# Kernel tuning notes

Hardware: AMD Instinct MI355X
Metric: run time of the kernel (lower is better)

The kernel has to match this reference:

```python
import jax, jax.numpy as jnp
import numpy as np

N_HEAD = 8
LN_EPS = 1e-5


def _layer_norm(x, g, b):
    mu = jnp.mean(x, axis=-1, keepdims=True)
    var = jnp.mean(jnp.square(x - mu), axis=-1, keepdims=True)
    return (x - mu) * jax.lax.rsqrt(var + LN_EPS) * g + b


def _pos_encoding(L, d, dtype):
    pos = jnp.arange(L, dtype=jnp.float32)[:, None]                      # [L,1]
    div = jnp.exp(jnp.arange(0, d, 2, dtype=jnp.float32) * (-np.log(10000.0) / d))  # [d/2]
    # interleave sin (even idx) / cos (odd idx)
    pe = jnp.stack([jnp.sin(pos * div), jnp.cos(pos * div)], axis=-1).reshape(L, d)
    return pe.astype(dtype)


def setup_inputs() -> dict:
    key = jax.random.key(0)
    B, L, D, F, NL = 256, 100, 512, 2048, 4
    ks = jax.random.split(key, 8)
    s = lambda fan_in: 1.0 / np.sqrt(fan_in)
    return {
        "x": jax.random.normal(ks[0], (B, L, D), dtype=jnp.float32),
        "mask": jnp.ones((B, L), dtype=jnp.int32),
        # weights stored as [in, out] (torch Linear weight transposed)
        "qkv_w": jax.random.uniform(ks[1], (NL, D, 3 * D), minval=-s(D), maxval=s(D)),
        "fc_w": jax.random.uniform(ks[2], (NL, D, D), minval=-s(D), maxval=s(D)),
        "fc_b": jnp.zeros((NL, D), dtype=jnp.float32),
        "ln1_g": jnp.ones((NL, D), dtype=jnp.float32),
        "ln1_b": jnp.zeros((NL, D), dtype=jnp.float32),
        "ln2_g": jnp.ones((NL, D), dtype=jnp.float32),
        "ln2_b": jnp.zeros((NL, D), dtype=jnp.float32),
        "ffn_w1": jax.random.uniform(ks[3], (NL, D, F), minval=-s(D), maxval=s(D)),
        "ffn_b1": jnp.zeros((NL, F), dtype=jnp.float32),
        "ffn_w2": jax.random.uniform(ks[4], (NL, F, D), minval=-s(F), maxval=s(F)),
        "ffn_b2": jnp.zeros((NL, D), dtype=jnp.float32),
    }


def _attn(x, mask, qkv_w, fc_w, fc_b):
    B, L, D = x.shape
    hd = D // N_HEAD
    qkv = x @ qkv_w                                      # [B,L,3D]
    q, k, v = jnp.split(qkv, 3, axis=-1)
    q = q.reshape(B, L, N_HEAD, hd).transpose(0, 2, 1, 3)   # [B,H,L,hd]
    k = k.reshape(B, L, N_HEAD, hd).transpose(0, 2, 1, 3)
    v = v.reshape(B, L, N_HEAD, hd).transpose(0, 2, 1, 3)
    scores = jnp.einsum("bhqd,bhkd->bhqk", q, k)          # scale=1 (scale=False)
    scores = jnp.where(mask[:, None, None, :] == 0, -jnp.inf, scores)
    attn = jax.nn.softmax(scores, axis=-1)
    out = jnp.einsum("bhqk,bhkd->bhqd", attn, v)
    out = out.transpose(0, 2, 1, 3).reshape(B, L, D)
    return out @ fc_w + fc_b


def reference(x, mask, qkv_w, fc_w, fc_b, ln1_g, ln1_b, ln2_g, ln2_b,
              ffn_w1, ffn_b1, ffn_w2, ffn_b2):
    B, L, D = x.shape
    pe = _pos_encoding(L, D, x.dtype)                     # [L,D]
    # pos_embed: x = x + (x + pe)  (dropout is identity at eval)
    x = x + (x + pe[None, :, :])
    n_layers = qkv_w.shape[0]
    for i in range(n_layers):  # post-norm (after_norm=True)
        res = x
        x = _attn(x, mask, qkv_w[i], fc_w[i], fc_b[i])
        x = _layer_norm(x + res, ln1_g[i], ln1_b[i])
        res = x
        h = jax.nn.relu(x @ ffn_w1[i] + ffn_b1[i])
        x = _layer_norm(res + (h @ ffn_w2[i] + ffn_b2[i]), ln2_g[i], ln2_b[i])
    return x
```

## Files before the change

### kernel.cpp

```cpp
#include <hip/hip_runtime.h>
#include <cstdint>
#include <cmath>


#define NLAYERS 4
#define BB 256
#define LL 100
#define DD 512
#define FF 2048
#define NH 8
#define HD 64
#define MM (BB*LL)
#define ATT_R 112
#define ATT_K 128

typedef __bf16 bf16;
typedef bf16 bf16x8 __attribute__((ext_vector_type(8)));
typedef bf16 bf16x4 __attribute__((ext_vector_type(4)));
typedef float f32x4 __attribute__((ext_vector_type(4)));

__device__ __forceinline__ void load16(const void* g, void* l) {
  __builtin_amdgcn_global_load_lds(
      (const __attribute__((address_space(1))) void*)g,
      (__attribute__((address_space(3))) void*)l, 16, 0, 0);
}

__global__ void pe_kernel(float* __restrict__ pe) {
  const int idx = blockIdx.x * 256 + threadIdx.x;
  if (idx >= LL * DD) return;
  const int l = idx >> 9, d = idx & 511;
  const int i = d >> 1;
  const float div = expf((float)(2 * i) * (-9.210340371976184f / 512.f));
  const float ang = (float)l * div;
  pe[idx] = (d & 1) ? cosf(ang) : sinf(ang);
}

__global__ __launch_bounds__(256) void x0_kernel(
    const float* __restrict__ xin, const float* __restrict__ pe,
    bf16* __restrict__ XB) {
  const size_t f = (size_t)blockIdx.x * 256 + threadIdx.x;
  const size_t e = f << 2;
  const int col  = (int)(e & 511);
  const int prow = (int)((e >> 9) % LL);
  const float4 xv = *(const float4*)(xin + e);
  const float4 pv = *(const float4*)(pe + (size_t)prow * DD + col);
  bf16x4 pk;
  pk[0] = (bf16)(2.f * xv.x + pv.x);
  pk[1] = (bf16)(2.f * xv.y + pv.y);
  pk[2] = (bf16)(2.f * xv.z + pv.z);
  pk[3] = (bf16)(2.f * xv.w + pv.w);
  *(bf16x4*)(XB + e) = pk;
}

__global__ void transpose_cast(const float* __restrict__ src, bf16* __restrict__ dst,
                               int K, int N) {
  __shared__ float tile[32][33];
  const int z = blockIdx.z;
  src += (size_t)z * K * N;
  dst += (size_t)z * K * N;
  const int k0 = blockIdx.y * 32, n0 = blockIdx.x * 32;
  const int tx = threadIdx.x, ty = threadIdx.y;
  #pragma unroll
  for (int i = 0; i < 32; i += 8)
    tile[ty + i][tx] = src[(size_t)(k0 + ty + i) * N + n0 + tx];
  __syncthreads();
  #pragma unroll
  for (int i = 0; i < 32; i += 8)
    dst[(size_t)(n0 + ty + i) * K + k0 + tx] = (bf16)tile[tx][ty + i];
}


__device__ __forceinline__ void stage_chunk(const bf16* __restrict__ src, int ldk,
                                            int grow0, int kt, bf16* chunk,
                                            int tid, int w) {
  const int rr = tid >> 3;
  const int cb = (tid & 7) ^ (rr & 7);
  const bf16* g = src + (size_t)(grow0 + rr) * ldk + (kt << 6) + (cb << 3);
  load16(g, chunk + (w << 9));
  load16(g + ((size_t)ldk << 6), chunk + 4096 + (w << 9));
}

__device__ __forceinline__ bf16x8 lds_frag(const bf16* chunk, int lrow, int cb) {
  return *(const bf16x8*)(chunk + (lrow << 6) + ((cb ^ (lrow & 7)) << 3));
}

template<int OUT_BF16, int RELU>
__global__ __launch_bounds__(512) void gemm256(
    const bf16* __restrict__ A, const bf16* __restrict__ Bt,
    const float* __restrict__ bias, void* __restrict__ Cv,
    int N, int K) {
  __shared__ __align__(16) bf16 sA[2][2][128 * 64];
  __shared__ __align__(16) bf16 sB[2][2][128 * 64];
  const int tid = threadIdx.x;
  const int w = tid >> 6, lane = tid & 63;
  const int wr = w >> 2, wc = w & 3;
  const int lr16 = lane & 15, lg = lane >> 4;
  const int NT = K >> 6;

  const int nwg = gridDim.x * gridDim.y;
  const int orig = blockIdx.y * gridDim.x + blockIdx.x;
  const int q = nwg >> 3, r = nwg & 7;
  const int xcd = orig & 7, lo = orig >> 3;
  const int swz = (xcd < r ? xcd * (q + 1) : r * (q + 1) + (xcd - r) * q) + lo;
  const int bn = (swz % gridDim.x) << 8;
  const int bm = (swz / gridDim.x) << 8;

  f32x4 acc[8][4] = {};
  bf16x8 Av[4][2], Bv0[2][2], Bv1[2][2];

  stage_chunk(A,  K, bm,       0, sA[0][0], tid, w);
  stage_chunk(Bt, K, bn,       0, sB[0][0], tid, w);
  stage_chunk(A,  K, bm + 128, 0, sA[0][1], tid, w);
  stage_chunk(Bt, K, bn + 128, 0, sB[0][1], tid, w);
  stage_chunk(A,  K, bm,       1, sA[1][0], tid, w);
  stage_chunk(Bt, K, bn,       1, sB[1][0], tid, w);

  for (int t = 0; t < NT; ++t) {
    const int b = t & 1;
    if (t < NT - 1) asm volatile("s_waitcnt vmcnt(4)" ::: "memory");
    else            asm volatile("s_waitcnt vmcnt(0)" ::: "memory");
    __builtin_amdgcn_s_barrier();

    #pragma unroll
    for (int m = 0; m < 4; ++m) {
      const int lrow = m * 32 + wr * 16 + lr16;
      Av[m][0] = lds_frag(sA[b][0], lrow, lg);
      Av[m][1] = lds_frag(sA[b][0], lrow, 4 + lg);
    }
    #pragma unroll
    for (int n = 0; n < 2; ++n) {
      const int lrow = n * 64 + wc * 16 + lr16;
      Bv0[n][0] = lds_frag(sB[b][0], lrow, lg);
      Bv0[n][1] = lds_frag(sB[b][0], lrow, 4 + lg);
    }
    if (t + 1 < NT) stage_chunk(A, K, bm + 128, t + 1, sA[b ^ 1][1], tid, w);
    __builtin_amdgcn_s_barrier();
    __builtin_amdgcn_s_setprio(1);
    #pragma unroll
    for (int m = 0; m < 4; ++m)
      #pragma unroll
      for (int n = 0; n < 2; ++n) {
        acc[m][n] = __builtin_amdgcn_mfma_f32_16x16x32_bf16(Av[m][0], Bv0[n][0], acc[m][n], 0, 0, 0);
        acc[m][n] = __builtin_amdgcn_mfma_f32_16x16x32_bf16(Av[m][1], Bv0[n][1], acc[m][n], 0, 0, 0);
      }
    __builtin_amdgcn_s_setprio(0);
    __builtin_amdgcn_s_barrier();

    #pragma unroll
    for (int n = 0; n < 2; ++n) {
      const int lrow = n * 64 + wc * 16 + lr16;
      Bv1[n][0] = lds_frag(sB[b][1], lrow, lg);
      Bv1[n][1] = lds_frag(sB[b][1], lrow, 4 + lg);
    }
    if (t + 1 < NT) stage_chunk(Bt, K, bn + 128, t + 1, sB[b ^ 1][1], tid, w);
    __builtin_amdgcn_s_barrier();
    __builtin_amdgcn_s_setprio(1);
    #pragma unroll
    for (int m = 0; m < 4; ++m)
      #pragma unroll
      for (int n = 0; n < 2; ++n) {
        acc[m][n + 2] = __builtin_amdgcn_mfma_f32_16x16x32_bf16(Av[m][0], Bv1[n][0], acc[m][n + 2], 0, 0, 0);
        acc[m][n + 2] = __builtin_amdgcn_mfma_f32_16x16x32_bf16(Av[m][1], Bv1[n][1], acc[m][n + 2], 0, 0, 0);
      }
    __builtin_amdgcn_s_setprio(0);
    __builtin_amdgcn_s_barrier();

    #pragma unroll
    for (int m = 0; m < 4; ++m) {
      const int lrow = m * 32 + wr * 16 + lr16;
      Av[m][0] = lds_frag(sA[b][1], lrow, lg);
      Av[m][1] = lds_frag(sA[b][1], lrow, 4 + lg);
    }
    if (t + 2 < NT) stage_chunk(A, K, bm, t + 2, sA[b][0], tid, w);
    __builtin_amdgcn_s_barrier();
    __builtin_amdgcn_s_setprio(1);
    #pragma unroll
    for (int m = 0; m < 4; ++m)
      #pragma unroll
      for (int n = 0; n < 2; ++n) {
        acc[m + 4][n] = __builtin_amdgcn_mfma_f32_16x16x32_bf16(Av[m][0], Bv0[n][0], acc[m + 4][n], 0, 0, 0);
        acc[m + 4][n] = __builtin_amdgcn_mfma_f32_16x16x32_bf16(Av[m][1], Bv0[n][1], acc[m + 4][n], 0, 0, 0);
      }
    __builtin_amdgcn_s_setprio(0);
    __builtin_amdgcn_s_barrier();

    if (t + 2 < NT) stage_chunk(Bt, K, bn, t + 2, sB[b][0], tid, w);
    __builtin_amdgcn_s_barrier();
    __builtin_amdgcn_s_setprio(1);
    #pragma unroll
    for (int m = 0; m < 4; ++m)
      #pragma unroll
      for (int n = 0; n < 2; ++n) {
        acc[m + 4][n + 2] = __builtin_amdgcn_mfma_f32_16x16x32_bf16(Av[m][0], Bv1[n][0], acc[m + 4][n + 2], 0, 0, 0);
        acc[m + 4][n + 2] = __builtin_amdgcn_mfma_f32_16x16x32_bf16(Av[m][1], Bv1[n][1], acc[m + 4][n + 2], 0, 0, 0);
      }
    __builtin_amdgcn_s_setprio(0);
  }

  const int g4 = (lane >> 4) << 2;
  #pragma unroll
  for (int n = 0; n < 4; ++n) {
    const int col = bn + n * 64 + wc * 16 + lr16;
    const float bvv = bias ? bias[col] : 0.f;
    #pragma unroll
    for (int m = 0; m < 8; ++m) {
      const int row = bm + m * 32 + wr * 16 + g4;
      #pragma unroll
      for (int j = 0; j < 4; ++j) {
        float v = acc[m][n][j] + bvv;
        if (RELU) v = fmaxf(v, 0.f);
        if (OUT_BF16) ((bf16*)Cv)[(size_t)(row + j) * N + col] = (bf16)v;
        else          ((float*)Cv)[(size_t)(row + j) * N + col] = v;
      }
    }
  }
}

__global__ __launch_bounds__(256) void attn_mfma(
    const bf16* __restrict__ qkv, const int* __restrict__ mask,
    bf16* __restrict__ aout) {
  __shared__ __align__(16) bf16 sQ[ATT_R * 64];
  __shared__ __align__(16) bf16 sK[ATT_R * 64];
  __shared__ __align__(16) bf16 sVt[64 * 136];
  __shared__ __align__(16) bf16 sP[ATT_R * ATT_K];
  __shared__ int sM[ATT_R];
  const int bh = blockIdx.x, b = bh >> 3, h = bh & 7;
  const int tid = threadIdx.x, w = tid >> 6, lane = tid & 63;
  const int lr = lane & 15;
  const int lk = (lane >> 4) << 3;
  const int g  = lane >> 4;

  for (int i = tid; i < ATT_R * 64 / 8; i += 256) { ((int4*)sQ)[i] = int4{0,0,0,0}; ((int4*)sK)[i] = int4{0,0,0,0}; }
  for (int i = tid; i < 64 * 136 / 8; i += 256) ((int4*)sVt)[i] = int4{0,0,0,0};
  for (int i = tid; i < ATT_R * ATT_K / 8; i += 256) ((int4*)sP)[i] = int4{0,0,0,0};
  __syncthreads();

  const bf16* base = qkv + (size_t)(b * LL) * (3 * DD) + h * HD;
  for (int c = tid; c < LL * 8; c += 256) {
    const int l = c >> 3, u = c & 7;
    const bf16x8 qv = *(const bf16x8*)(base + (size_t)l * (3 * DD) + u * 8);
    const bf16x8 kv = *(const bf16x8*)(base + (size_t)l * (3 * DD) + DD + u * 8);
    const bf16x8 vv = *(const bf16x8*)(base + (size_t)l * (3 * DD) + 2 * DD + u * 8);
    const int qb = (l * 128 + u * 16) ^ ((l & 7) << 4);
    *(bf16x8*)((char*)sQ + qb) = qv;
    *(bf16x8*)((char*)sK + qb) = kv;
    #pragma unroll
    for (int j = 0; j < 8; ++j) sVt[(u * 8 + j) * 136 + l] = vv[j];
  }
  if (tid < ATT_R) sM[tid] = (tid < LL) ? mask[b * LL + tid] : 0;
  __syncthreads();

  #pragma unroll
  for (int fi = 0; fi < 2; ++fi) {
    const int fm = w + fi * 4;
    if (fm >= 7) continue;
    const int ar = fm * 16 + lr;
    const int abase = ar * 128;
    const int aswz = (ar & 7) << 4;
    const bf16x8 a0 = *(const bf16x8*)((char*)sQ + ((abase + lk * 2) ^ aswz));
    const bf16x8 a1 = *(const bf16x8*)((char*)sQ + ((abase + 64 + lk * 2) ^ aswz));
    f32x4 s[7];
    #pragma unroll
    for (int fn = 0; fn < 7; ++fn) {
      const int br = fn * 16 + lr;
      const int bswz = (br & 7) << 4;
      const bf16x8 b0 = *(const bf16x8*)((char*)sK + ((br * 128 + lk * 2) ^ bswz));
      const bf16x8 b1 = *(const bf16x8*)((char*)sK + ((br * 128 + 64 + lk * 2) ^ bswz));
      f32x4 acc = {};
      acc = __builtin_amdgcn_mfma_f32_16x16x32_bf16(a0, b0, acc, 0, 0, 0);
      acc = __builtin_amdgcn_mfma_f32_16x16x32_bf16(a1, b1, acc, 0, 0, 0);
      s[fn] = acc;
    }
    #pragma unroll
    for (int fn = 0; fn < 7; ++fn) {
      if (sM[fn * 16 + lr] == 0) {
        s[fn][0] = -INFINITY; s[fn][1] = -INFINITY;
        s[fn][2] = -INFINITY; s[fn][3] = -INFINITY;
      }
    }
    float sm[4];
    #pragma unroll
    for (int j = 0; j < 4; ++j) {
      float m = s[0][j];
      #pragma unroll
      for (int fn = 1; fn < 7; ++fn) m = fmaxf(m, s[fn][j]);
      #pragma unroll
      for (int off = 1; off < 16; off <<= 1) m = fmaxf(m, __shfl_xor(m, off, 64));
      float t = 0.f;
      #pragma unroll
      for (int fn = 0; fn < 7; ++fn) { const float p = __expf(s[fn][j] - m); s[fn][j] = p; t += p; }
      #pragma unroll
      for (int off = 1; off < 16; off <<= 1) t += __shfl_xor(t, off, 64);
      sm[j] = 1.f / t;
    }
    #pragma unroll
    for (int fn = 0; fn < 7; ++fn) {
      const int k = fn * 16 + lr;
      #pragma unroll
      for (int j = 0; j < 4; ++j) {
        const int rr = fm * 16 + 4 * g + j;
        const int byte = (rr * 256 + k * 2) ^ ((rr & 7) << 4);
        *(bf16*)((char*)sP + byte) = (bf16)(s[fn][j] * sm[j]);
      }
    }
  }
  __syncthreads();

  bf16x8 bV[4];
  #pragma unroll
  for (int ks = 0; ks < 4; ++ks)
    bV[ks] = *(const bf16x8*)((char*)sVt + ((w * 16 + lr) * 272 + ks * 64 + lk * 2));
  #pragma unroll
  for (int fm = 0; fm < 7; ++fm) {
    f32x4 acc = {};
    const int ar = fm * 16 + lr;
    const int aswz = (ar & 7) << 4;
    #pragma unroll
    for (int ks = 0; ks < 4; ++ks) {
      const bf16x8 aP = *(const bf16x8*)((char*)sP + ((ar * 256 + ks * 64 + lk * 2) ^ aswz));
      acc = __builtin_amdgcn_mfma_f32_16x16x32_bf16(aP, bV[ks], acc, 0, 0, 0);
    }
    const int d = h * HD + w * 16 + lr;
    #pragma unroll
    for (int j = 0; j < 4; ++j) {
      const int qr = fm * 16 + 4 * g + j;
      if (qr < LL) aout[(size_t)(b * LL + qr) * DD + d] = (bf16)acc[j];
    }
  }
}

template<int WRITE_F32>
__global__ __launch_bounds__(64) void ln_kernel(
    const float* __restrict__ Y, const bf16* __restrict__ RES,
    const float* __restrict__ g, const float* __restrict__ bt,
    bf16* __restrict__ XB, float* __restrict__ XF) {
  const int row = blockIdx.x;
  const int lane = threadIdx.x;
  const size_t base = (size_t)row * DD + lane * 8;
  const float4 a0 = *(const float4*)(Y + base);
  const float4 a1 = *(const float4*)(Y + base + 4);
  const bf16x8 rv = *(const bf16x8*)(RES + base);
  float z[8];
  z[0] = a0.x + (float)rv[0]; z[1] = a0.y + (float)rv[1];
  z[2] = a0.z + (float)rv[2]; z[3] = a0.w + (float)rv[3];
  z[4] = a1.x + (float)rv[4]; z[5] = a1.y + (float)rv[5];
  z[6] = a1.z + (float)rv[6]; z[7] = a1.w + (float)rv[7];
  float s = 0.f, s2 = 0.f;
  #pragma unroll
  for (int j = 0; j < 8; ++j) { s += z[j]; s2 = fmaf(z[j], z[j], s2); }
  #pragma unroll
  for (int off = 32; off > 0; off >>= 1) {
    s  += __shfl_xor(s, off, 64);
    s2 += __shfl_xor(s2, off, 64);
  }
  const float mu = s * (1.f / 512.f);
  const float var = s2 * (1.f / 512.f) - mu * mu;
  const float inv = rsqrtf(var + 1e-5f);
  const int c = lane * 8;
  const float4 g0 = *(const float4*)(g + c),  g1 = *(const float4*)(g + c + 4);
  const float4 b0 = *(const float4*)(bt + c), b1 = *(const float4*)(bt + c + 4);
  float ov[8];
  ov[0] = (z[0] - mu) * inv * g0.x + b0.x; ov[1] = (z[1] - mu) * inv * g0.y + b0.y;
  ov[2] = (z[2] - mu) * inv * g0.z + b0.z; ov[3] = (z[3] - mu) * inv * g0.w + b0.w;
  ov[4] = (z[4] - mu) * inv * g1.x + b1.x; ov[5] = (z[5] - mu) * inv * g1.y + b1.y;
  ov[6] = (z[6] - mu) * inv * g1.z + b1.z; ov[7] = (z[7] - mu) * inv * g1.w + b1.w;
  bf16x8 pk;
  #pragma unroll
  for (int j = 0; j < 8; ++j) pk[j] = (bf16)ov[j];
  *(bf16x8*)(XB + base) = pk;
  if (WRITE_F32) {
    *(float4*)(XF + base)     = make_float4(ov[0], ov[1], ov[2], ov[3]);
    *(float4*)(XF + base + 4) = make_float4(ov[4], ov[5], ov[6], ov[7]);
  }
}

extern "C" void kernel_launch(void* const* d_in, const int* in_sizes, int n_in,
                              void* d_out, int out_size, void* d_ws, size_t ws_size,
                              hipStream_t stream) {
  const float* x_in   = (const float*)d_in[0];
  const int*   mask   = (const int*)d_in[1];
  const float* qkv_w  = (const float*)d_in[2];
  const float* fc_w   = (const float*)d_in[3];
  const float* fc_b   = (const float*)d_in[4];
  const float* ln1_g  = (const float*)d_in[5];
  const float* ln1_b  = (const float*)d_in[6];
  const float* ln2_g  = (const float*)d_in[7];
  const float* ln2_b  = (const float*)d_in[8];
  const float* ffn_w1 = (const float*)d_in[9];
  const float* ffn_b1 = (const float*)d_in[10];
  const float* ffn_w2 = (const float*)d_in[11];
  const float* ffn_b2 = (const float*)d_in[12];

  char* ws = (char*)d_ws;
  size_t off = 0;
  auto alloc = [&](size_t bytes) -> void* {
    off = (off + 255) & ~(size_t)255;
    void* p = ws + off;
    off += bytes;
    return p;
  };
  bf16*  XB   = (bf16*) alloc((size_t)MM * DD * 2);
  bf16*  BIGB = (bf16*) alloc((size_t)MM * FF * 2);
  float* PE   = (float*)alloc((size_t)LL * DD * 4);
  bf16*  WQKV = (bf16*) alloc((size_t)NLAYERS * DD * 3 * DD * 2);
  bf16*  WFC  = (bf16*) alloc((size_t)NLAYERS * DD * DD * 2);
  bf16*  W1T  = (bf16*) alloc((size_t)NLAYERS * DD * FF * 2);
  bf16*  W2T  = (bf16*) alloc((size_t)NLAYERS * FF * DD * 2);
  bf16*  AOUT = BIGB + (size_t)MM * (3 * DD);
  float* Y    = (float*)d_out;
  (void)ws_size; (void)in_sizes; (void)n_in; (void)out_size;

  pe_kernel<<<200, 256, 0, stream>>>(PE);
  transpose_cast<<<dim3(48, 16, NLAYERS), dim3(32, 8), 0, stream>>>(qkv_w,  WQKV, 512, 1536);
  transpose_cast<<<dim3(16, 16, NLAYERS), dim3(32, 8), 0, stream>>>(fc_w,   WFC,  512, 512);
  transpose_cast<<<dim3(64, 16, NLAYERS), dim3(32, 8), 0, stream>>>(ffn_w1, W1T,  512, 2048);
  transpose_cast<<<dim3(16, 64, NLAYERS), dim3(32, 8), 0, stream>>>(ffn_w2, W2T,  2048, 512);
  x0_kernel<<<12800, 256, 0, stream>>>(x_in, PE, XB);

  for (int i = 0; i < NLAYERS; ++i) {
    gemm256<1, 0><<<dim3(6, 100), 512, 0, stream>>>(
        XB, WQKV + (size_t)i * DD * 3 * DD, nullptr, BIGB, 3 * DD, DD);
    attn_mfma<<<BB * NH, 256, 0, stream>>>(BIGB, mask, AOUT);
    gemm256<0, 0><<<dim3(2, 100), 512, 0, stream>>>(
        AOUT, WFC + (size_t)i * DD * DD, fc_b + i * DD, Y, DD, DD);
    ln_kernel<0><<<MM, 64, 0, stream>>>(Y, XB, ln1_g + i * DD, ln1_b + i * DD, XB, nullptr);
    gemm256<1, 1><<<dim3(8, 100), 512, 0, stream>>>(
        XB, W1T + (size_t)i * DD * FF, ffn_b1 + i * FF, BIGB, FF, DD);
    gemm256<0, 0><<<dim3(2, 100), 512, 0, stream>>>(
        BIGB, W2T + (size_t)i * FF * DD, ffn_b2 + i * DD, Y, DD, FF);
    if (i == NLAYERS - 1)
      ln_kernel<1><<<MM, 64, 0, stream>>>(Y, XB, ln2_g + i * DD, ln2_b + i * DD,
                                          XB, (float*)d_out);
    else
      ln_kernel<0><<<MM, 64, 0, stream>>>(Y, XB, ln2_g + i * DD, ln2_b + i * DD, XB, nullptr);
  }
}
```

Baseline: 1.236 ms.

## Add 128x128 tiled GEMM for N=512 projections and batch LN rows per block

Adds a gemm128 kernel with 128x128 tiles, 256 threads, double-buffered LDS staging and an XCD-aware block swizzle. It is used for the fc and FFN-down GEMMs (N=512), which launched only 200 blocks with the 256-wide tile and underfilled the GPU. The LayerNorm kernel now handles four rows per 256-thread block instead of one row per 64-thread block, to cut launch and scheduling overhead. Smaller tiles mean less reuse per loaded byte and more total global traffic for A and B.

Result: slower. 1.315 ms (+6.4%).

```diff
diff --git a/kernel.cpp b/kernel.cpp
--- a/kernel.cpp
+++ b/kernel.cpp
@@ -69,7 +69,6 @@
     dst[(size_t)(n0 + ty + i) * K + k0 + tx] = (bf16)tile[tx][ty + i];
 }
 
-
 __device__ __forceinline__ void stage_chunk(const bf16* __restrict__ src, int ldk,
                                             int grow0, int kt, bf16* chunk,
                                             int tid, int w) {
@@ -208,6 +207,156 @@
       #pragma unroll
       for (int j = 0; j < 4; ++j) {
         float v = acc[m][n][j] + bvv;
+        if (RELU) v = fmaxf(v, 0.f);
+        if (OUT_BF16) ((bf16*)Cv)[(size_t)(row + j) * N + col] = (bf16)v;
+        else          ((float*)Cv)[(size_t)(row + j) * N + col] = v;
+      }
+    }
+  }
+}
+
+__device__ __forceinline__ void stage64(const bf16*& pa, const bf16*& pb,
+                                        bf16* dst, int w) {
+  load16(pa, dst + (w << 9));
+  load16(pb, dst + 2048 + (w << 9));
+  pa += 64; pb += 64;
+}
+
+template<int OUT_BF16, int RELU>
+__global__ __launch_bounds__(256, 2) void gemm128(
+    const bf16* __restrict__ A, const bf16* __restrict__ Bt,
+    const float* __restrict__ bias, void* __restrict__ Cv,
+    int N, int K) {
+  __shared__ __align__(16) bf16 sA[2][2][64 * 64];
+  __shared__ __align__(16) bf16 sB[2][2][64 * 64];
+  const int tid = threadIdx.x;
+  const int w = tid >> 6, lane = tid & 63;
+  const int wr = w >> 1, wc = w & 1;
+  const int lr16 = lane & 15, lg = lane >> 4;
+  const int NT = K >> 6;
+
+  const int nwg = gridDim.x * gridDim.y;
+  const int orig = blockIdx.y * gridDim.x + blockIdx.x;
+  const int q = nwg >> 3, r = nwg & 7;
+  const int xcd = orig & 7, lo = orig >> 3;
+  const int swz = (xcd < r ? xcd * (q + 1) : r * (q + 1) + (xcd - r) * q) + lo;
+  const int bn = (swz % gridDim.x) << 7;
+  const int bm = (swz / gridDim.x) << 7;
+
+  auto mksrc = [&](const bf16* base, int grow0, int i) -> const bf16* {
+    const int p = i * 256 + tid;
+    const int prow = p >> 3;
+    const int cbl = (p & 7) ^ (prow & 7);
+    return base + (size_t)(grow0 + prow) * K + (cbl << 3);
+  };
+  const bf16* pA0a = mksrc(A, bm, 0);        const bf16* pA0b = mksrc(A, bm, 1);
+  const bf16* pA1a = mksrc(A, bm + 64, 0);   const bf16* pA1b = mksrc(A, bm + 64, 1);
+  const bf16* pB0a = mksrc(Bt, bn, 0);       const bf16* pB0b = mksrc(Bt, bn, 1);
+  const bf16* pB1a = mksrc(Bt, bn + 64, 0);  const bf16* pB1b = mksrc(Bt, bn + 64, 1);
+
+  f32x4 acc[4][4] = {};
+  bf16x8 Am[2][2], Bn0[2][2], Bn1[2][2];
+
+  stage64(pA0a, pA0b, sA[0][0], w);
+  stage64(pB0a, pB0b, sB[0][0], w);
+  stage64(pA1a, pA1b, sA[0][1], w);
+  stage64(pB1a, pB1b, sB[0][1], w);
+  stage64(pA0a, pA0b, sA[1][0], w);
+  stage64(pB0a, pB0b, sB[1][0], w);
+
+  for (int t = 0; t < NT; ++t) {
+    const int b = t & 1;
+    if (t < NT - 1) asm volatile("s_waitcnt vmcnt(4)" ::: "memory");
+    else            asm volatile("s_waitcnt vmcnt(0)" ::: "memory");
+    __builtin_amdgcn_s_barrier();
+
+    #pragma unroll
+    for (int m = 0; m < 2; ++m) {
+      const int lrow = m * 32 + wr * 16 + lr16;
+      Am[m][0] = lds_frag(sA[b][0], lrow, lg);
+      Am[m][1] = lds_frag(sA[b][0], lrow, 4 + lg);
+    }
+    #pragma unroll
+    for (int n = 0; n < 2; ++n) {
+      const int lrow = n * 32 + wc * 16 + lr16;
+      Bn0[n][0] = lds_frag(sB[b][0], lrow, lg);
+      Bn0[n][1] = lds_frag(sB[b][0], lrow, 4 + lg);
+    }
+    if (t + 1 < NT) stage64(pA1a, pA1b, sA[b ^ 1][1], w);
+    __builtin_amdgcn_s_barrier();
+    __builtin_amdgcn_s_setprio(1);
+    #pragma unroll
+    for (int m = 0; m < 2; ++m)
+      #pragma unroll
+      for (int n = 0; n < 2; ++n) {
+        acc[m][n] = __builtin_amdgcn_mfma_f32_16x16x32_bf16(Am[m][0], Bn0[n][0], acc[m][n], 0, 0, 0);
+        acc[m][n] = __builtin_amdgcn_mfma_f32_16x16x32_bf16(Am[m][1], Bn0[n][1], acc[m][n], 0, 0, 0);
+      }
+    __builtin_amdgcn_s_setprio(0);
+    __builtin_amdgcn_s_barrier();
+
+    #pragma unroll
+    for (int n = 0; n < 2; ++n) {
+      const int lrow = n * 32 + wc * 16 + lr16;
+      Bn1[n][0] = lds_frag(sB[b][1], lrow, lg);
+      Bn1[n][1] = lds_frag(sB[b][1], lrow, 4 + lg);
+    }
+    if (t + 1 < NT) stage64(pB1a, pB1b, sB[b ^ 1][1], w);
+    __builtin_amdgcn_s_barrier();
+    __builtin_amdgcn_s_setprio(1);
+    #pragma unroll
+    for (int m = 0; m < 2; ++m)
+      #pragma unroll
+      for (int n = 0; n < 2; ++n) {
+        acc[m][n + 2] = __builtin_amdgcn_mfma_f32_16x16x32_bf16(Am[m][0], Bn1[n][0], acc[m][n + 2], 0, 0, 0);
+        acc[m][n + 2] = __builtin_amdgcn_mfma_f32_16x16x32_bf16(Am[m][1], Bn1[n][1], acc[m][n + 2], 0, 0, 0);
+      }
+    __builtin_amdgcn_s_setprio(0);
+    __builtin_amdgcn_s_barrier();
+
+    #pragma unroll
+    for (int m = 0; m < 2; ++m) {
+      const int lrow = m * 32 + wr * 16 + lr16;
+      Am[m][0] = lds_frag(sA[b][1], lrow, lg);
+      Am[m][1] = lds_frag(sA[b][1], lrow, 4 + lg);
+    }
+    if (t + 2 < NT) stage64(pA0a, pA0b, sA[b][0], w);
+    __builtin_amdgcn_s_barrier();
+    __builtin_amdgcn_s_setprio(1);
+    #pragma unroll
+    for (int m = 0; m < 2; ++m)
+      #pragma unroll
+      for (int n = 0; n < 2; ++n) {
+        acc[m + 2][n] = __builtin_amdgcn_mfma_f32_16x16x32_bf16(Am[m][0], Bn0[n][0], acc[m + 2][n], 0, 0, 0);
+        acc[m + 2][n] = __builtin_amdgcn_mfma_f32_16x16x32_bf16(Am[m][1], Bn0[n][1], acc[m + 2][n], 0, 0, 0);
+      }
+    __builtin_amdgcn_s_setprio(0);
+    __builtin_amdgcn_s_barrier();
+
+    if (t + 2 < NT) stage64(pB0a, pB0b, sB[b][0], w);
+    __builtin_amdgcn_s_barrier();
+    __builtin_amdgcn_s_setprio(1);
+    #pragma unroll
+    for (int m = 0; m < 2; ++m)
+      #pragma unroll
+      for (int n = 0; n < 2; ++n) {
+        acc[m + 2][n + 2] = __builtin_amdgcn_mfma_f32_16x16x32_bf16(Am[m][0], Bn1[n][0], acc[m + 2][n + 2], 0, 0, 0);
+        acc[m + 2][n + 2] = __builtin_amdgcn_mfma_f32_16x16x32_bf16(Am[m][1], Bn1[n][1], acc[m + 2][n + 2], 0, 0, 0);
+      }
+    __builtin_amdgcn_s_setprio(0);
+  }
+
+  const int g4 = (lane >> 4) << 2;
+  #pragma unroll
+  for (int ni = 0; ni < 4; ++ni) {
+    const int col = bn + (ni >> 1) * 64 + (ni & 1) * 32 + wc * 16 + lr16;
+    const float bvv = bias ? bias[col] : 0.f;
+    #pragma unroll
+    for (int mi = 0; mi < 4; ++mi) {
+      const int row = bm + (mi >> 1) * 64 + (mi & 1) * 32 + wr * 16 + g4;
+      #pragma unroll
+      for (int j = 0; j < 4; ++j) {
+        float v = acc[mi][ni][j] + bvv;
         if (RELU) v = fmaxf(v, 0.f);
         if (OUT_BF16) ((bf16*)Cv)[(size_t)(row + j) * N + col] = (bf16)v;
         else          ((float*)Cv)[(size_t)(row + j) * N + col] = v;
@@ -330,12 +479,12 @@
 }
 
 template<int WRITE_F32>
-__global__ __launch_bounds__(64) void ln_kernel(
+__global__ __launch_bounds__(256) void ln_kernel(
     const float* __restrict__ Y, const bf16* __restrict__ RES,
     const float* __restrict__ g, const float* __restrict__ bt,
     bf16* __restrict__ XB, float* __restrict__ XF) {
-  const int row = blockIdx.x;
-  const int lane = threadIdx.x;
+  const int row = blockIdx.x * 4 + (threadIdx.x >> 6);
+  const int lane = threadIdx.x & 63;
   const size_t base = (size_t)row * DD + lane * 8;
   const float4 a0 = *(const float4*)(Y + base);
   const float4 a1 = *(const float4*)(Y + base + 4);
@@ -421,17 +570,17 @@
     gemm256<1, 0><<<dim3(6, 100), 512, 0, stream>>>(
         XB, WQKV + (size_t)i * DD * 3 * DD, nullptr, BIGB, 3 * DD, DD);
     attn_mfma<<<BB * NH, 256, 0, stream>>>(BIGB, mask, AOUT);
-    gemm256<0, 0><<<dim3(2, 100), 512, 0, stream>>>(
+    gemm128<0, 0><<<dim3(4, 200), 256, 0, stream>>>(
         AOUT, WFC + (size_t)i * DD * DD, fc_b + i * DD, Y, DD, DD);
-    ln_kernel<0><<<MM, 64, 0, stream>>>(Y, XB, ln1_g + i * DD, ln1_b + i * DD, XB, nullptr);
+    ln_kernel<0><<<MM / 4, 256, 0, stream>>>(Y, XB, ln1_g + i * DD, ln1_b + i * DD, XB, nullptr);
     gemm256<1, 1><<<dim3(8, 100), 512, 0, stream>>>(
         XB, W1T + (size_t)i * DD * FF, ffn_b1 + i * FF, BIGB, FF, DD);
-    gemm256<0, 0><<<dim3(2, 100), 512, 0, stream>>>(
+    gemm128<0, 0><<<dim3(4, 200), 256, 0, stream>>>(
         BIGB, W2T + (size_t)i * FF * DD, ffn_b2 + i * DD, Y, DD, FF);
     if (i == NLAYERS - 1)
-      ln_kernel<1><<<MM, 64, 0, stream>>>(Y, XB, ln2_g + i * DD, ln2_b + i * DD,
-                                          XB, (float*)d_out);
+      ln_kernel<1><<<MM / 4, 256, 0, stream>>>(Y, XB, ln2_g + i * DD, ln2_b + i * DD,
+                                               XB, (float*)d_out);
     else
-      ln_kernel<0><<<MM, 64, 0, stream>>>(Y, XB, ln2_g + i * DD, ln2_b + i * DD, XB, nullptr);
-  }
-}
+      ln_kernel<0><<<MM / 4, 256, 0, stream>>>(Y, XB, ln2_g + i * DD, ln2_b + i * DD, XB, nullptr);
+  }
+}
```

## Fuse output-projection and FFN2 GEMMs with residual add and LayerNorm

Applied to the files above, without the earlier changes.

Adds a gemm_ln kernel in which each 512-thread block computes a full 128x512 row tile, so it owns every column of its rows and can apply bias, residual add and LayerNorm in its epilogue. This replaces the fp32 Y round trip and the separate ln_kernel launches after the fc and ffn_w2 GEMMs. In exchange, only 200 blocks are launched for these GEMMs, which may underfill the GPU. The epilogue reads and writes XB in place, which is safe only because each block touches just its own rows. A dead extra LDS load was also added in attention, which is probably harmless.

Result: slower. 1.396 ms (+13.0%).

```diff
diff --git a/kernel.cpp b/kernel.cpp
--- a/kernel.cpp
+++ b/kernel.cpp
@@ -69,7 +69,6 @@
     dst[(size_t)(n0 + ty + i) * K + k0 + tx] = (bf16)tile[tx][ty + i];
 }
 
-
 __device__ __forceinline__ void stage_chunk(const bf16* __restrict__ src, int ldk,
                                             int grow0, int kt, bf16* chunk,
                                             int tid, int w) {
@@ -211,6 +210,169 @@
         if (RELU) v = fmaxf(v, 0.f);
         if (OUT_BF16) ((bf16*)Cv)[(size_t)(row + j) * N + col] = (bf16)v;
         else          ((float*)Cv)[(size_t)(row + j) * N + col] = v;
+      }
+    }
+  }
+}
+
+template<int WRITE_F32>
+__global__ __launch_bounds__(512) void gemm_ln(
+    const bf16* __restrict__ A, const bf16* __restrict__ Bt,
+    const float* __restrict__ bias, const bf16* __restrict__ RES,
+    const float* __restrict__ lng, const float* __restrict__ lnb,
+    bf16* __restrict__ XB, float* __restrict__ XF, int K) {
+  __shared__ __align__(16) bf16 sA[2][128 * 32];
+  __shared__ __align__(16) bf16 sB[2][512 * 32];
+  const int tid = threadIdx.x;
+  const int w = tid >> 6, lane = tid & 63;
+  const int wc = w;
+  const int lr16 = lane & 15, lg = lane >> 4;
+  const int NT = K >> 5;
+
+  const int q = gridDim.x >> 3;
+  const int swz = (blockIdx.x & 7) * q + (blockIdx.x >> 3);
+  const int bm = swz << 7;
+
+  const int rr = tid >> 2;
+  const int cbl = (tid & 3) ^ (rr & 3);
+  const bf16* gA  = A  + (size_t)(bm + rr) * K + (cbl << 3);
+  const bf16* gB0 = Bt + (size_t)(0   + rr) * K + (cbl << 3);
+  const bf16* gB1 = Bt + (size_t)(128 + rr) * K + (cbl << 3);
+  const bf16* gB2 = Bt + (size_t)(256 + rr) * K + (cbl << 3);
+  const bf16* gB3 = Bt + (size_t)(384 + rr) * K + (cbl << 3);
+
+  f32x4 acc[8][4] = {};
+  bf16x8 Af[4], Bf[4];
+
+  load16(gA,       sA[0] + (w << 9));
+  load16(gB0,      sB[0] + 0 * 4096 + (w << 9));
+  load16(gB1,      sB[0] + 1 * 4096 + (w << 9));
+  load16(gB2,      sB[0] + 2 * 4096 + (w << 9));
+  load16(gB3,      sB[0] + 3 * 4096 + (w << 9));
+  load16(gB0 + 32, sB[1] + 0 * 4096 + (w << 9));
+  load16(gB1 + 32, sB[1] + 1 * 4096 + (w << 9));
+  load16(gB2 + 32, sB[1] + 2 * 4096 + (w << 9));
+  load16(gB3 + 32, sB[1] + 3 * 4096 + (w << 9));
+
+  for (int t = 0; t < NT; ++t) {
+    const int pb = t & 1;
+    const bf16* bufA = sA[pb];
+    const bf16* bufB = sB[pb];
+    if (t < NT - 1) asm volatile("s_waitcnt vmcnt(4)" ::: "memory");
+    else            asm volatile("s_waitcnt vmcnt(0)" ::: "memory");
+    __builtin_amdgcn_s_barrier();
+
+    #pragma unroll
+    for (int m = 0; m < 4; ++m) {
+      const int row = m * 16 + lr16;
+      Af[m] = *(const bf16x8*)&bufA[row * 32 + ((lg ^ (row & 3)) << 3)];
+    }
+    #pragma unroll
+    for (int n = 0; n < 4; ++n) {
+      const int row = wc * 64 + n * 16 + lr16;
+      Bf[n] = *(const bf16x8*)&bufB[row * 32 + ((lg ^ (row & 3)) << 3)];
+    }
+    if (t + 1 < NT) load16(gA + (t + 1) * 32, sA[pb ^ 1] + (w << 9));
+    __builtin_amdgcn_s_barrier();
+    __builtin_amdgcn_s_setprio(1);
+    #pragma unroll
+    for (int m = 0; m < 4; ++m)
+      #pragma unroll
+      for (int n = 0; n < 4; ++n)
+        acc[m][n] = __builtin_amdgcn_mfma_f32_16x16x32_bf16(Af[m], Bf[n], acc[m][n], 0, 0, 0);
+    __builtin_amdgcn_s_setprio(0);
+    __builtin_amdgcn_s_barrier();
+
+    #pragma unroll
+    for (int m = 0; m < 4; ++m) {
+      const int row = (m + 4) * 16 + lr16;
+      Af[m] = *(const bf16x8*)&bufA[row * 32 + ((lg ^ (row & 3)) << 3)];
+    }
+    if (t + 2 < NT) {
+      const int ko = (t + 2) * 32;
+      load16(gB0 + ko, sB[pb] + 0 * 4096 + (w << 9));
+      load16(gB1 + ko, sB[pb] + 1 * 4096 + (w << 9));
+      load16(gB2 + ko, sB[pb] + 2 * 4096 + (w << 9));
+      load16(gB3 + ko, sB[pb] + 3 * 4096 + (w << 9));
+    }
+    __builtin_amdgcn_s_barrier();
+    __builtin_amdgcn_s_setprio(1);
+    #pragma unroll
+    for (int m = 0; m < 4; ++m)
+      #pragma unroll
+      for (int n = 0; n < 4; ++n)
+        acc[m + 4][n] = __builtin_amdgcn_mfma_f32_16x16x32_bf16(Af[m], Bf[n], acc[m + 4][n], 0, 0, 0);
+    __builtin_amdgcn_s_setprio(0);
+  }
+
+  __syncthreads();
+  float* redS = (float*)sA;
+  float* muS  = (float*)sB;
+
+  int colv[4];
+  #pragma unroll
+  for (int n = 0; n < 4; ++n) colv[n] = wc * 64 + n * 16 + lr16;
+
+  #pragma unroll
+  for (int m = 0; m < 8; ++m) {
+    #pragma unroll
+    for (int j = 0; j < 4; ++j) {
+      const int row = m * 16 + (lg << 2) + j;
+      const size_t gr = (size_t)(bm + row) * DD;
+      #pragma unroll
+      for (int n = 0; n < 4; ++n)
+        acc[m][n][j] += bias[colv[n]] + (float)RES[gr + colv[n]];
+    }
+  }
+  #pragma unroll
+  for (int m = 0; m < 8; ++m) {
+    #pragma unroll
+    for (int j = 0; j < 4; ++j) {
+      float s  = acc[m][0][j] + acc[m][1][j] + acc[m][2][j] + acc[m][3][j];
+      float s2 = acc[m][0][j] * acc[m][0][j] + acc[m][1][j] * acc[m][1][j]
+               + acc[m][2][j] * acc[m][2][j] + acc[m][3][j] * acc[m][3][j];
+      #pragma unroll
+      for (int off = 1; off < 16; off <<= 1) {
+        s  += __shfl_xor(s, off, 64);
+        s2 += __shfl_xor(s2, off, 64);
+      }
+      if (lr16 == 0) {
+        const int row = m * 16 + (lg << 2) + j;
+        redS[row * 16 + wc * 2]     = s;
+        redS[row * 16 + wc * 2 + 1] = s2;
+      }
+    }
+  }
+  __syncthreads();
+  if (tid < 128) {
+    float s = 0.f, s2 = 0.f;
+    #pragma unroll
+    for (int wv = 0; wv < 8; ++wv) {
+      s  += redS[tid * 16 + wv * 2];
+      s2 += redS[tid * 16 + wv * 2 + 1];
+    }
+    const float mu  = s * (1.f / 512.f);
+    const float var = s2 * (1.f / 512.f) - mu * mu;
+    muS[tid]       = mu;
+    muS[128 + tid] = rsqrtf(var + 1e-5f);
+  }
+  __syncthreads();
+  float gmv[4], btv[4];
+  #pragma unroll
+  for (int n = 0; n < 4; ++n) { gmv[n] = lng[colv[n]]; btv[n] = lnb[colv[n]]; }
+  #pragma unroll
+  for (int m = 0; m < 8; ++m) {
+    #pragma unroll
+    for (int j = 0; j < 4; ++j) {
+      const int row = m * 16 + (lg << 2) + j;
+      const float mu  = muS[row];
+      const float inv = muS[128 + row];
+      const size_t gr = (size_t)(bm + row) * DD;
+      #pragma unroll
+      for (int n = 0; n < 4; ++n) {
+        const float o = (acc[m][n][j] - mu) * inv * gmv[n] + btv[n];
+        XB[gr + colv[n]] = (bf16)o;
+        if (WRITE_F32) XF[gr + colv[n]] = o;
       }
     }
   }
@@ -317,8 +479,10 @@
     const int aswz = (ar & 7) << 4;
     #pragma unroll
     for (int ks = 0; ks < 4; ++ks) {
-      const bf16x8 aP = *(const bf16x8*)((char*)sP + ((ar * 256 + ks * 64 + lk * 2) ^ aswz));
-      acc = __builtin_amdgcn_mfma_f32_16x16x32_bf16(aP, bV[ks], acc, 0, 0, 0);
+      const bf16x8 aP = *(const bf16x8*)((char*)sVt + 0);
+      (void)aP;
+      const bf16x8 aP2 = *(const bf16x8*)((char*)sP + ((ar * 256 + ks * 64 + lk * 2) ^ aswz));
+      acc = __builtin_amdgcn_mfma_f32_16x16x32_bf16(aP2, bV[ks], acc, 0, 0, 0);
     }
     const int d = h * HD + w * 16 + lr;
     #pragma unroll
@@ -326,51 +490,6 @@
       const int qr = fm * 16 + 4 * g + j;
       if (qr < LL) aout[(size_t)(b * LL + qr) * DD + d] = (bf16)acc[j];
     }
-  }
-}
-
-template<int WRITE_F32>
-__global__ __launch_bounds__(64) void ln_kernel(
-    const float* __restrict__ Y, const bf16* __restrict__ RES,
-    const float* __restrict__ g, const float* __restrict__ bt,
-    bf16* __restrict__ XB, float* __restrict__ XF) {
-  const int row = blockIdx.x;
-  const int lane = threadIdx.x;
-  const size_t base = (size_t)row * DD + lane * 8;
-  const float4 a0 = *(const float4*)(Y + base);
-  const float4 a1 = *(const float4*)(Y + base + 4);
-  const bf16x8 rv = *(const bf16x8*)(RES + base);
-  float z[8];
-  z[0] = a0.x + (float)rv[0]; z[1] = a0.y + (float)rv[1];
-  z[2] = a0.z + (float)rv[2]; z[3] = a0.w + (float)rv[3];
-  z[4] = a1.x + (float)rv[4]; z[5] = a1.y + (float)rv[5];
-  z[6] = a1.z + (float)rv[6]; z[7] = a1.w + (float)rv[7];
-  float s = 0.f, s2 = 0.f;
-  #pragma unroll
-  for (int j = 0; j < 8; ++j) { s += z[j]; s2 = fmaf(z[j], z[j], s2); }
-  #pragma unroll
-  for (int off = 32; off > 0; off >>= 1) {
-    s  += __shfl_xor(s, off, 64);
-    s2 += __shfl_xor(s2, off, 64);
-  }
-  const float mu = s * (1.f / 512.f);
-  const float var = s2 * (1.f / 512.f) - mu * mu;
-  const float inv = rsqrtf(var + 1e-5f);
-  const int c = lane * 8;
-  const float4 g0 = *(const float4*)(g + c),  g1 = *(const float4*)(g + c + 4);
-  const float4 b0 = *(const float4*)(bt + c), b1 = *(const float4*)(bt + c + 4);
-  float ov[8];
-  ov[0] = (z[0] - mu) * inv * g0.x + b0.x; ov[1] = (z[1] - mu) * inv * g0.y + b0.y;
-  ov[2] = (z[2] - mu) * inv * g0.z + b0.z; ov[3] = (z[3] - mu) * inv * g0.w + b0.w;
-  ov[4] = (z[4] - mu) * inv * g1.x + b1.x; ov[5] = (z[5] - mu) * inv * g1.y + b1.y;
-  ov[6] = (z[6] - mu) * inv * g1.z + b1.z; ov[7] = (z[7] - mu) * inv * g1.w + b1.w;
-  bf16x8 pk;
-  #pragma unroll
-  for (int j = 0; j < 8; ++j) pk[j] = (bf16)ov[j];
-  *(bf16x8*)(XB + base) = pk;
-  if (WRITE_F32) {
-    *(float4*)(XF + base)     = make_float4(ov[0], ov[1], ov[2], ov[3]);
-    *(float4*)(XF + base + 4) = make_float4(ov[4], ov[5], ov[6], ov[7]);
   }
 }
 
@@ -407,7 +526,6 @@
   bf16*  W1T  = (bf16*) alloc((size_t)NLAYERS * DD * FF * 2);
   bf16*  W2T  = (bf16*) alloc((size_t)NLAYERS * FF * DD * 2);
   bf16*  AOUT = BIGB + (size_t)MM * (3 * DD);
-  float* Y    = (float*)d_out;
   (void)ws_size; (void)in_sizes; (void)n_in; (void)out_size;
 
   pe_kernel<<<200, 256, 0, stream>>>(PE);
@@ -421,17 +539,18 @@
     gemm256<1, 0><<<dim3(6, 100), 512, 0, stream>>>(
         XB, WQKV + (size_t)i * DD * 3 * DD, nullptr, BIGB, 3 * DD, DD);
     attn_mfma<<<BB * NH, 256, 0, stream>>>(BIGB, mask, AOUT);
-    gemm256<0, 0><<<dim3(2, 100), 512, 0, stream>>>(
-        AOUT, WFC + (size_t)i * DD * DD, fc_b + i * DD, Y, DD, DD);
-    ln_kernel<0><<<MM, 64, 0, stream>>>(Y, XB, ln1_g + i * DD, ln1_b + i * DD, XB, nullptr);
+    gemm_ln<0><<<200, 512, 0, stream>>>(
+        AOUT, WFC + (size_t)i * DD * DD, fc_b + i * DD, XB,
+        ln1_g + i * DD, ln1_b + i * DD, XB, nullptr, DD);
     gemm256<1, 1><<<dim3(8, 100), 512, 0, stream>>>(
         XB, W1T + (size_t)i * DD * FF, ffn_b1 + i * FF, BIGB, FF, DD);
-    gemm256<0, 0><<<dim3(2, 100), 512, 0, stream>>>(
-        BIGB, W2T + (size_t)i * FF * DD, ffn_b2 + i * DD, Y, DD, FF);
     if (i == NLAYERS - 1)
-      ln_kernel<1><<<MM, 64, 0, stream>>>(Y, XB, ln2_g + i * DD, ln2_b + i * DD,
-                                          XB, (float*)d_out);
+      gemm_ln<1><<<200, 512, 0, stream>>>(
+          BIGB, W2T + (size_t)i * FF * DD, ffn_b2 + i * DD, XB,
+          ln2_g + i * DD, ln2_b + i * DD, XB, (float*)d_out, FF);
     else
-      ln_kernel<0><<<MM, 64, 0, stream>>>(Y, XB, ln2_g + i * DD, ln2_b + i * DD, XB, nullptr);
-  }
-}
+      gemm_ln<0><<<200, 512, 0, stream>>>(
+          BIGB, W2T + (size_t)i * FF * DD, ffn_b2 + i * DD, XB,
+          ln2_g + i * DD, ln2_b + i * DD, XB, nullptr, FF);
+  }
+}
```

## Add 128x128-tile GEMM with XCD swizzle for N=512 GEMMs, batch LN rows

Applied to the files above, without the earlier changes.

Adds a new gemm128 kernel with 128x128 tiles, 256 threads, double-buffered LDS staging and an XCD-aware block swizzle. It replaces the 256-tile GEMM for the two N=512 projections (attention output fc and FFN down), which launched only 200 workgroups and so under-filled the GPU. The layer-norm kernel now handles four rows per 256-thread block instead of one row per 64-thread block, cutting launch and scheduling overhead. The smaller tiles reuse less data per load and raise total global traffic.

After: 1.199 ms. 1.03x faster.

```diff
diff --git a/kernel.cpp b/kernel.cpp
--- a/kernel.cpp
+++ b/kernel.cpp
@@ -69,7 +69,6 @@
     dst[(size_t)(n0 + ty + i) * K + k0 + tx] = (bf16)tile[tx][ty + i];
 }
 
-
 __device__ __forceinline__ void stage_chunk(const bf16* __restrict__ src, int ldk,
                                             int grow0, int kt, bf16* chunk,
                                             int tid, int w) {
@@ -205,6 +204,105 @@
     #pragma unroll
     for (int m = 0; m < 8; ++m) {
       const int row = bm + m * 32 + wr * 16 + g4;
+      #pragma unroll
+      for (int j = 0; j < 4; ++j) {
+        float v = acc[m][n][j] + bvv;
+        if (RELU) v = fmaxf(v, 0.f);
+        if (OUT_BF16) ((bf16*)Cv)[(size_t)(row + j) * N + col] = (bf16)v;
+        else          ((float*)Cv)[(size_t)(row + j) * N + col] = v;
+      }
+    }
+  }
+}
+
+__device__ __forceinline__ void stage4(const bf16* g, size_t r32, bf16* chunk, int w) {
+  load16(g,            chunk + (w << 9));
+  load16(g + r32,      chunk + 2048 + (w << 9));
+  load16(g + 2 * r32,  chunk + 4096 + (w << 9));
+  load16(g + 3 * r32,  chunk + 6144 + (w << 9));
+}
+
+template<int OUT_BF16, int RELU>
+__global__ __launch_bounds__(256, 2) void gemm128(
+    const bf16* __restrict__ A, const bf16* __restrict__ Bt,
+    const float* __restrict__ bias, void* __restrict__ Cv,
+    int N, int K) {
+  __shared__ __align__(16) bf16 sA[2][128 * 64];
+  __shared__ __align__(16) bf16 sB[2][128 * 64];
+  const int tid = threadIdx.x;
+  const int w = tid >> 6, lane = tid & 63;
+  const int wr = w >> 1, wc = w & 1;
+  const int lr16 = lane & 15, lg = lane >> 4;
+  const int NT = K >> 6;
+
+  const int nwg = gridDim.x * gridDim.y;
+  const int orig = blockIdx.y * gridDim.x + blockIdx.x;
+  const int q = nwg >> 3, r = nwg & 7;
+  const int xcd = orig & 7, lo = orig >> 3;
+  const int swz = (xcd < r ? xcd * (q + 1) : r * (q + 1) + (xcd - r) * q) + lo;
+  const int bn = (swz % gridDim.x) << 7;
+  const int bm = (swz / gridDim.x) << 7;
+
+  const int rr0 = tid >> 3;
+  const int cb  = (tid & 7) ^ (rr0 & 7);
+  const bf16* gA = A  + (size_t)(bm + rr0) * K + (cb << 3);
+  const bf16* gB = Bt + (size_t)(bn + rr0) * K + (cb << 3);
+  const size_t r32 = (size_t)32 * K;
+
+  f32x4 acc[4][4] = {};
+  bf16x8 Af[4][2], Bf[4][2];
+
+  stage4(gA,      r32, sA[0], w);
+  stage4(gB,      r32, sB[0], w);
+  stage4(gA + 64, r32, sA[1], w);
+  stage4(gB + 64, r32, sB[1], w);
+
+  for (int t = 0; t < NT; ++t) {
+    const int cur = t & 1;
+    if (t < NT - 1) asm volatile("s_waitcnt vmcnt(8)" ::: "memory");
+    else            asm volatile("s_waitcnt vmcnt(0)" ::: "memory");
+    __builtin_amdgcn_s_barrier();
+
+    #pragma unroll
+    for (int m = 0; m < 4; ++m) {
+      const int lrow = wr * 64 + m * 16 + lr16;
+      Af[m][0] = lds_frag(sA[cur], lrow, lg);
+      Af[m][1] = lds_frag(sA[cur], lrow, 4 + lg);
+    }
+    #pragma unroll
+    for (int n = 0; n < 4; ++n) {
+      const int lrow = wc * 64 + n * 16 + lr16;
+      Bf[n][0] = lds_frag(sB[cur], lrow, lg);
+      Bf[n][1] = lds_frag(sB[cur], lrow, 4 + lg);
+    }
+    __builtin_amdgcn_s_barrier();
+
+    if (t + 2 < NT) stage4(gA + (size_t)(t + 2) * 64, r32, sA[cur], w);
+    __builtin_amdgcn_s_setprio(1);
+    #pragma unroll
+    for (int m = 0; m < 4; ++m)
+      #pragma unroll
+      for (int n = 0; n < 4; ++n)
+        acc[m][n] = __builtin_amdgcn_mfma_f32_16x16x32_bf16(Af[m][0], Bf[n][0], acc[m][n], 0, 0, 0);
+    __builtin_amdgcn_s_setprio(0);
+    if (t + 2 < NT) stage4(gB + (size_t)(t + 2) * 64, r32, sB[cur], w);
+    __builtin_amdgcn_s_setprio(1);
+    #pragma unroll
+    for (int m = 0; m < 4; ++m)
+      #pragma unroll
+      for (int n = 0; n < 4; ++n)
+        acc[m][n] = __builtin_amdgcn_mfma_f32_16x16x32_bf16(Af[m][1], Bf[n][1], acc[m][n], 0, 0, 0);
+    __builtin_amdgcn_s_setprio(0);
+  }
+
+  const int g4 = (lane >> 4) << 2;
+  #pragma unroll
+  for (int n = 0; n < 4; ++n) {
+    const int col = bn + wc * 64 + n * 16 + lr16;
+    const float bvv = bias ? bias[col] : 0.f;
+    #pragma unroll
+    for (int m = 0; m < 4; ++m) {
+      const int row = bm + wr * 64 + m * 16 + g4;
       #pragma unroll
       for (int j = 0; j < 4; ++j) {
         float v = acc[m][n][j] + bvv;
@@ -330,12 +428,12 @@
 }
 
 template<int WRITE_F32>
-__global__ __launch_bounds__(64) void ln_kernel(
+__global__ __launch_bounds__(256) void ln_kernel(
     const float* __restrict__ Y, const bf16* __restrict__ RES,
     const float* __restrict__ g, const float* __restrict__ bt,
     bf16* __restrict__ XB, float* __restrict__ XF) {
-  const int row = blockIdx.x;
-  const int lane = threadIdx.x;
+  const int row = blockIdx.x * 4 + (threadIdx.x >> 6);
+  const int lane = threadIdx.x & 63;
   const size_t base = (size_t)row * DD + lane * 8;
   const float4 a0 = *(const float4*)(Y + base);
   const float4 a1 = *(const float4*)(Y + base + 4);
@@ -421,17 +519,17 @@
     gemm256<1, 0><<<dim3(6, 100), 512, 0, stream>>>(
         XB, WQKV + (size_t)i * DD * 3 * DD, nullptr, BIGB, 3 * DD, DD);
     attn_mfma<<<BB * NH, 256, 0, stream>>>(BIGB, mask, AOUT);
-    gemm256<0, 0><<<dim3(2, 100), 512, 0, stream>>>(
+    gemm128<0, 0><<<dim3(4, 200), 256, 0, stream>>>(
         AOUT, WFC + (size_t)i * DD * DD, fc_b + i * DD, Y, DD, DD);
-    ln_kernel<0><<<MM, 64, 0, stream>>>(Y, XB, ln1_g + i * DD, ln1_b + i * DD, XB, nullptr);
+    ln_kernel<0><<<MM / 4, 256, 0, stream>>>(Y, XB, ln1_g + i * DD, ln1_b + i * DD, XB, nullptr);
     gemm256<1, 1><<<dim3(8, 100), 512, 0, stream>>>(
         XB, W1T + (size_t)i * DD * FF, ffn_b1 + i * FF, BIGB, FF, DD);
-    gemm256<0, 0><<<dim3(2, 100), 512, 0, stream>>>(
+    gemm128<0, 0><<<dim3(4, 200), 256, 0, stream>>>(
         BIGB, W2T + (size_t)i * FF * DD, ffn_b2 + i * DD, Y, DD, FF);
     if (i == NLAYERS - 1)
-      ln_kernel<1><<<MM, 64, 0, stream>>>(Y, XB, ln2_g + i * DD, ln2_b + i * DD,
-                                          XB, (float*)d_out);
+      ln_kernel<1><<<MM / 4, 256, 0, stream>>>(Y, XB, ln2_g + i * DD, ln2_b + i * DD,
+                                               XB, (float*)d_out);
     else
-      ln_kernel<0><<<MM, 64, 0, stream>>>(Y, XB, ln2_g + i * DD, ln2_b + i * DD, XB, nullptr);
-  }
-}
+      ln_kernel<0><<<MM / 4, 256, 0, stream>>>(Y, XB, ln2_g + i * DD, ln2_b + i * DD, XB, nullptr);
+  }
+}
```
